# Kernel optimization log

Hardware: AMD Instinct MI355X
Metric: run time of the kernel (lower is better)

## Reference

```python
import jax, jax.numpy as jnp
import numpy as np

WH, WW = 7, 7
N = WH * WW
DIM = 384
HEADS = 12
NW = 64          # windows per image
B_ = 2048        # batch * NW


def _relative_position_index():
    ch, cw = np.meshgrid(np.arange(WH), np.arange(WW), indexing='ij')
    coords = np.stack([ch, cw]).reshape(2, -1)                      # [2, N]
    rel = coords[:, :, None] - coords[:, None, :]                   # [2, N, N]
    rel = rel.transpose(1, 2, 0)
    rel[:, :, 0] += WH - 1
    rel[:, :, 1] += WW - 1
    rel[:, :, 0] *= 2 * WW - 1
    return jnp.asarray(rel.sum(-1), dtype=jnp.int32)                # [N, N]


def setup_inputs() -> dict:
    key = jax.random.key(0)
    ks = jax.random.split(key, 7)
    return {
        'x': jax.random.normal(ks[0], (B_, N, DIM), dtype=jnp.float32),
        'qkv_w': jax.random.normal(ks[1], (3 * DIM, DIM), dtype=jnp.float32) * 0.02,
        'qkv_b': jax.random.normal(ks[2], (3 * DIM,), dtype=jnp.float32) * 0.02,
        'proj_w': jax.random.normal(ks[3], (DIM, DIM), dtype=jnp.float32) * 0.02,
        'proj_b': jax.random.normal(ks[4], (DIM,), dtype=jnp.float32) * 0.02,
        'bias_table': jax.random.normal(ks[5], ((2 * WH - 1) * (2 * WW - 1), HEADS), dtype=jnp.float32) * 0.02,
        'mask': jax.random.normal(ks[6], (NW, N, N), dtype=jnp.float32),
        'rel_idx': _relative_position_index(),
    }


def reference(x, qkv_w, qkv_b, proj_w, proj_b, bias_table, mask, rel_idx):
    B_, n, C = x.shape
    H = HEADS
    hd = C // H
    scale = hd ** (-0.5)

    qkv = x @ qkv_w.T + qkv_b                                        # [B_, N, 3C]
    qkv = qkv.reshape(B_, n, 3, H, hd).transpose(2, 0, 3, 1, 4)      # [3, B_, H, N, hd]
    q, k, v = qkv[0], qkv[1], qkv[2]

    attn = jnp.einsum('bhqd,bhkd->bhqk', q * scale, k)               # [B_, H, N, N]

    rpb = bias_table[rel_idx.reshape(-1)].reshape(n, n, H)           # gather [N, N, H]
    attn = attn + rpb.transpose(2, 0, 1)[None]                       # [B_, H, N, N]

    nW = mask.shape[0]
    attn = attn.reshape(B_ // nW, nW, H, n, n) + mask[None, :, None]
    attn = attn.reshape(B_, H, n, n)
    attn = jax.nn.softmax(attn, axis=-1)

    out = jnp.einsum('bhqk,bhkd->bhqd', attn, v)                     # [B_, H, N, hd]
    out = out.transpose(0, 2, 1, 3).reshape(B_, n, C)
    return out @ proj_w.T + proj_b
```

## Files before the change

kernel.cpp:

```cpp
#include <hip/hip_runtime.h>
#include <hip/hip_bf16.h>
#include <cstdint>
#include <cstddef>

#define NTOK 49
#define DIM 384
#define KDIM 384
#define HEADS 12
#define HD 32
#define BATCH 2048
#define MROWS (BATCH * NTOK)

typedef unsigned short u16;
typedef __bf16 bf16x8 __attribute__((ext_vector_type(8)));
typedef unsigned short u16x8 __attribute__((ext_vector_type(8)));
typedef float f32x4 __attribute__((ext_vector_type(4)));

__device__ __forceinline__ u16 f2b(float f) {
  union { float f; unsigned u; } v; v.f = f;
  unsigned r = v.u + 0x7fffu + ((v.u >> 16) & 1u);
  return (u16)(r >> 16);
}

__device__ __forceinline__ bf16x8 ld_bf8(const u16* p) {
  u16x8 u = *(const u16x8*)p;
  return __builtin_bit_cast(bf16x8, u);
}

__device__ __forceinline__ void gload_lds16(const void* g, void* l) {
  __builtin_amdgcn_global_load_lds(
      (const __attribute__((address_space(1))) unsigned*)g,
      (__attribute__((address_space(3))) unsigned*)l, 16, 0, 0);
}

__global__ __launch_bounds__(256) void k_prep(const float* __restrict__ x,
                                              u16* __restrict__ xb,
                                              const float* __restrict__ qkv_w,
                                              u16* __restrict__ wqkvb,
                                              const float* __restrict__ proj_w,
                                              u16* __restrict__ wprojb,
                                              const float* __restrict__ bias_table,
                                              const float* __restrict__ mask,
                                              const int* __restrict__ rel_idx,
                                              float* __restrict__ rpbm) {
  int blk = blockIdx.x;
  if (blk < 38208) {
    const float* in;
    u16* out;
    int i;
    if (blk < 37632) {
      in = x; out = xb; i = blk * 256 + threadIdx.x;
    } else if (blk < 38064) {
      in = qkv_w; out = wqkvb; i = (blk - 37632) * 256 + threadIdx.x;
    } else {
      in = proj_w; out = wprojb; i = (blk - 38064) * 256 + threadIdx.x;
    }
    float4 v = ((const float4*)in)[i];
    ushort4 o;
    o.x = f2b(v.x); o.y = f2b(v.y); o.z = f2b(v.z); o.w = f2b(v.w);
    ((ushort4*)out)[i] = o;
  } else {
    int idx = (blk - 38208) * 256 + threadIdx.x;
    int r  = idx & 3;
    int l  = (idx >> 2) & 63;
    int ni = (idx >> 8) & 3;
    int mi = (idx >> 10) & 3;
    int w  = (idx >> 12) & 63;
    int h  = idx >> 18;
    int kk = mi * 16 + (l >> 4) * 4 + r;
    int qq = ni * 16 + (l & 15);
    float v = -1e30f;
    if (kk < NTOK && qq < NTOK)
      v = bias_table[rel_idx[qq * NTOK + kk] * HEADS + h] +
          mask[(w * NTOK + qq) * NTOK + kk];
    rpbm[idx] = v;
  }
}

template <int OUT_BF16, int NCOLS, int NTN, int GD8>
__global__ __launch_bounds__(512, 4) void k_gemm256(const u16* __restrict__ A,
                                                    const u16* __restrict__ B,
                                                    const float* __restrict__ bias,
                                                    void* __restrict__ Cv) {
  __shared__ u16 sh[36864];
  int bid = blockIdx.x;
  int tile = (bid & 7) * GD8 + (bid >> 3);
  int mt = tile / NTN, nt = tile - mt * NTN;
  long m0 = (long)mt * 256;
  int n0 = nt * 128;
  int tid = threadIdx.x;
  int lane = tid & 63, wid = tid >> 6;
  int wr = (wid >> 1) * 64, wc = (wid & 1) * 64;
  int c = lane & 15, g = lane >> 4;
  int gsw = (g ^ ((c >> 1) & 3)) * 8;

  int srow = wid * 16 + (lane >> 2);
  int scol = ((lane & 3) ^ ((lane >> 3) & 3)) * 8;
  const u16* gA = A + (m0 + srow) * (long)KDIM + scol;
  const u16* gB = B + (long)(n0 + srow) * KDIM + scol;
  int lrow = srow, lseg = (lane & 3) * 8;

  f32x4 acc[4][4] = {};
  bf16x8 af[4], bfr[4];

#define STAGE256(BUF, KT)                                                      \
  {                                                                            \
    u16* As_ = sh + (BUF) * 12288;                                             \
    u16* Bs_ = As_ + 8192;                                                     \
    gload_lds16(gA + (KT), &As_[lrow * 32 + lseg]);                            \
    gload_lds16(gA + (KT) + 128L * KDIM, &As_[(lrow + 128) * 32 + lseg]);      \
    gload_lds16(gB + (KT), &Bs_[lrow * 32 + lseg]);                            \
  }

#define FRAGREAD(BUF)                                                          \
  {                                                                            \
    const u16* As = sh + (BUF) * 12288;                                        \
    const u16* Bs = As + 8192;                                                 \
    _Pragma("unroll") for (int i = 0; i < 4; ++i) {                            \
      af[i]  = ld_bf8(&As[(wr + i * 16 + c) * 32 + gsw]);                      \
      bfr[i] = ld_bf8(&Bs[(wc + i * 16 + c) * 32 + gsw]);                      \
    }                                                                          \
  }

#define MFMA_CL                                                                \
  __builtin_amdgcn_s_setprio(1);                                               \
  _Pragma("unroll") for (int mi = 0; mi < 4; ++mi)                             \
  _Pragma("unroll") for (int ni = 0; ni < 4; ++ni)                             \
      acc[mi][ni] = __builtin_amdgcn_mfma_f32_16x16x32_bf16(                   \
          af[mi], bfr[ni], acc[mi][ni], 0, 0, 0);                              \
  __builtin_amdgcn_s_setprio(0);

#define GITER(T, NV)                                                           \
  {                                                                            \
    MFMA_CL;                                                                   \
    asm volatile("s_waitcnt vmcnt(" #NV ")" ::: "memory");                     \
    __builtin_amdgcn_s_barrier();                                              \
    __builtin_amdgcn_sched_barrier(0);                                         \
    if ((T) + 3 < 12) STAGE256((T) % 3, ((T) + 3) * 32);                       \
    FRAGREAD(((T) + 1) % 3);                                                   \
  }

  STAGE256(0, 0);
  STAGE256(1, 32);
  STAGE256(2, 64);
  asm volatile("s_waitcnt vmcnt(6)" ::: "memory");
  __builtin_amdgcn_s_barrier();
  __builtin_amdgcn_sched_barrier(0);
  FRAGREAD(0);

  GITER(0, 3)  GITER(1, 3)  GITER(2, 3)  GITER(3, 3)
  GITER(4, 3)  GITER(5, 3)  GITER(6, 3)  GITER(7, 3)
  GITER(8, 3)  GITER(9, 3)  GITER(10, 0)
  { MFMA_CL; }
  __builtin_amdgcn_s_barrier();
#undef GITER
#undef MFMA_CL
#undef FRAGREAD
#undef STAGE256

  if (OUT_BF16) {
    u16* C = (u16*)Cv;
#pragma unroll
    for (int mi = 0; mi < 4; ++mi)
#pragma unroll
      for (int ni = 0; ni < 4; ++ni) {
        int col = wc + ni * 16 + c;
        float bv = bias[n0 + col];
#pragma unroll
        for (int r = 0; r < 4; ++r) {
          int row = wr + mi * 16 + g * 4 + r;
          sh[row * 128 + col] = f2b(acc[mi][ni][r] + bv);
        }
      }
    __syncthreads();
#pragma unroll
    for (int rep = 0; rep < 8; ++rep) {
      int idx = rep * 4096 + tid * 8;
      int row = idx >> 7, col = idx & 127;
      int grow = (int)m0 + row;
      int b = grow / 49, tok = grow - b * 49;
      int gcol = n0 + col;
      int t = gcol / 384;
      int hc = gcol - t * 384;
      int h = hc >> 5, d0 = hc & 31;
      size_t off = (((size_t)(t * 12 + h) * BATCH + b) * 49 + tok) * 32 + d0;
      *(u16x8*)(C + off) = *(const u16x8*)&sh[idx];
    }
  } else {
    float* C = (float*)Cv;
    float* shf = (float*)sh;
#pragma unroll
    for (int chunk = 0; chunk < 2; ++chunk) {
      __syncthreads();
      if ((wid >> 2) == chunk) {
#pragma unroll
        for (int mi = 0; mi < 4; ++mi)
#pragma unroll
          for (int ni = 0; ni < 4; ++ni) {
            int col = wc + ni * 16 + c;
            float bv = bias[n0 + col];
#pragma unroll
            for (int r = 0; r < 4; ++r) {
              int lr = ((wid >> 1) & 1) * 64 + mi * 16 + g * 4 + r;
              shf[lr * 128 + col] = acc[mi][ni][r] + bv;
            }
          }
      }
      __syncthreads();
#pragma unroll
      for (int rep = 0; rep < 8; ++rep) {
        int idx = rep * 2048 + tid * 4;
        int row = idx >> 7, col = idx & 127;
        *(float4*)(C + (m0 + chunk * 128 + row) * NCOLS + n0 + col) =
            *(const float4*)&shf[idx];
      }
    }
  }
}

__global__ __launch_bounds__(256) void k_attn(const u16* __restrict__ qkv,
                                              const float* __restrict__ rpbmT,
                                              u16* __restrict__ attnout) {
  __shared__ u16 P_lds[4][64 * 64];
  __shared__ u16 vT_lds[4][32 * 64];
  int lane = threadIdx.x & 63, wid = threadIdx.x >> 6;
  int blk = blockIdx.x;
  int w = blk / 96;
  int rr = blk - w * 96;
  int j = rr / 3;
  int hb = rr - j * 3;
  int b = j * 64 + w;
  int h = hb * 4 + wid;
  int c = lane & 15, g = lane >> 4;

  const u16* qh = qkv + ((size_t)(h)*BATCH + b) * (49 * 32);
  const u16* kh = qkv + ((size_t)(12 + h) * BATCH + b) * (49 * 32);
  const u16* vh = qkv + ((size_t)(24 + h) * BATCH + b) * (49 * 32);

  u16x8 vv[4];
#pragma unroll
  for (int t = 0; t < 4; ++t) {
    int idx = t * 64 + lane;
    int jj = idx >> 2, d0 = (idx & 3) * 8;
    int jr = jj < NTOK ? jj : NTOK - 1;
    vv[t] = *(const u16x8*)(vh + jr * 32 + d0);
  }
  bf16x8 kf[4], qf[4];
#pragma unroll
  for (int mi = 0; mi < 4; ++mi) {
    int row = mi * 16 + c; if (row > NTOK - 1) row = NTOK - 1;
    kf[mi] = ld_bf8(kh + row * 32 + g * 8);
  }
#pragma unroll
  for (int nj = 0; nj < 4; ++nj) {
    int row = nj * 16 + c; if (row > NTOK - 1) row = NTOK - 1;
    qf[nj] = ld_bf8(qh + row * 32 + g * 8);
  }

  u16* vt = vT_lds[wid];
#pragma unroll
  for (int t = 0; t < 4; ++t) {
    int idx = t * 64 + lane;
    int jj = idx >> 2, d0 = (idx & 3) * 8;
#pragma unroll
    for (int dd = 0; dd < 8; ++dd) {
      int d = d0 + dd;
      int byte = (d * 128 + jj * 2) ^ ((d & 7) << 4);
      *(u16*)((char*)vt + byte) = (u16)vv[t][dd];
    }
  }

  f32x4 s[4][4];
  f32x4 zf = {0.f, 0.f, 0.f, 0.f};
#pragma unroll
  for (int mi = 0; mi < 4; ++mi)
#pragma unroll
    for (int nj = 0; nj < 4; ++nj)
      s[mi][nj] = __builtin_amdgcn_mfma_f32_16x16x32_bf16(kf[mi], qf[nj], zf,
                                                          0, 0, 0);

  const float scale = 0.17677669529663687f;
  const f32x4* rp = (const f32x4*)(rpbmT + ((size_t)(h * 64 + w)) * 4096);
#pragma unroll
  for (int mi = 0; mi < 4; ++mi)
#pragma unroll
    for (int nj = 0; nj < 4; ++nj) {
      f32x4 rv = rp[(mi * 4 + nj) * 64 + lane];
#pragma unroll
      for (int r = 0; r < 4; ++r)
        s[mi][nj][r] = s[mi][nj][r] * scale + rv[r];
    }

  float inv[4];
#pragma unroll
  for (int nj = 0; nj < 4; ++nj) {
    float mx = s[0][nj][0];
#pragma unroll
    for (int mi = 0; mi < 4; ++mi)
#pragma unroll
      for (int r = 0; r < 4; ++r)
        mx = fmaxf(mx, s[mi][nj][r]);
    mx = fmaxf(mx, __shfl_xor(mx, 16));
    mx = fmaxf(mx, __shfl_xor(mx, 32));
    float sum = 0.f;
#pragma unroll
    for (int mi = 0; mi < 4; ++mi)
#pragma unroll
      for (int r = 0; r < 4; ++r) {
        float p = __expf(s[mi][nj][r] - mx);
        s[mi][nj][r] = p;
        sum += p;
      }
    sum += __shfl_xor(sum, 16);
    sum += __shfl_xor(sum, 32);
    inv[nj] = __builtin_amdgcn_rcpf(sum);
  }

  u16* pl = P_lds[wid];
#pragma unroll
  for (int mi = 0; mi < 4; ++mi)
#pragma unroll
    for (int nj = 0; nj < 4; ++nj) {
      unsigned w0, w1;
      asm("v_cvt_pk_bf16_f32 %0, %1, %2"
          : "=v"(w0) : "v"(s[mi][nj][0]), "v"(s[mi][nj][1]));
      asm("v_cvt_pk_bf16_f32 %0, %1, %2"
          : "=v"(w1) : "v"(s[mi][nj][2]), "v"(s[mi][nj][3]));
      int q = nj * 16 + c;
      int byte = (q * 128 + (mi * 16 + g * 4) * 2) ^ ((c & 7) << 4);
      uint2 val; val.x = w0; val.y = w1;
      *(uint2*)((char*)pl + byte) = val;
    }
  asm volatile("s_waitcnt lgkmcnt(0)" ::: "memory");
  __builtin_amdgcn_sched_barrier(0);

  f32x4 o[2][4] = {};
#pragma unroll
  for (int ks = 0; ks < 2; ++ks) {
    bf16x8 vb[2];
#pragma unroll
    for (int mi2 = 0; mi2 < 2; ++mi2) {
      int d = mi2 * 16 + c;
      int byte = (d * 128 + ks * 64 + g * 16) ^ ((d & 7) << 4);
      vb[mi2] = __builtin_bit_cast(bf16x8, *(const u16x8*)((const char*)vt + byte));
    }
#pragma unroll
    for (int nj = 0; nj < 4; ++nj) {
      int q = nj * 16 + c;
      int byte = (q * 128 + (ks * 32 + g * 8) * 2) ^ ((c & 7) << 4);
      bf16x8 pb = __builtin_bit_cast(bf16x8, *(const u16x8*)((const char*)pl + byte));
#pragma unroll
      for (int mi2 = 0; mi2 < 2; ++mi2)
        o[mi2][nj] = __builtin_amdgcn_mfma_f32_16x16x32_bf16(vb[mi2], pb,
                                                             o[mi2][nj], 0, 0, 0);
    }
  }

  u16* obase = attnout + (size_t)b * (NTOK * DIM) + h * HD;
#pragma unroll
  for (int mi2 = 0; mi2 < 2; ++mi2)
#pragma unroll
    for (int nj = 0; nj < 4; ++nj) {
      int q = nj * 16 + c;
      if (q < NTOK) {
#pragma unroll
        for (int r = 0; r < 4; ++r)
          obase[(size_t)q * DIM + mi2 * 16 + g * 4 + r] =
              f2b(o[mi2][nj][r] * inv[nj]);
      }
    }
}

extern "C" void kernel_launch(void* const* d_in, const int* in_sizes, int n_in,
                              void* d_out, int out_size, void* d_ws, size_t ws_size,
                              hipStream_t stream) {
  const float* x       = (const float*)d_in[0];
  const float* qkv_w   = (const float*)d_in[1];
  const float* qkv_b   = (const float*)d_in[2];
  const float* proj_w  = (const float*)d_in[3];
  const float* proj_b  = (const float*)d_in[4];
  const float* bias_tb = (const float*)d_in[5];
  const float* mask    = (const float*)d_in[6];
  const int*   rel_idx = (const int*)d_in[7];
  float* out = (float*)d_out;

  char* ws = (char*)d_ws;
  u16*   xb      = (u16*)(ws + 0);
  u16*   wqkvb   = (u16*)(ws + 77070336);
  u16*   wprojb  = (u16*)(ws + 77955072);
  float* rpbm    = (float*)(ws + 78249984);
  u16*   qkv     = (u16*)(ws + 90832896);
  u16*   attnout = (u16*)(ws + 322043904);

  k_prep<<<50496, 256, 0, stream>>>(x, xb, qkv_w, wqkvb, proj_w, wprojb,
                                    bias_tb, mask, rel_idx, rpbm);

  k_gemm256<1, 1152, 9, 441><<<3528, 512, 0, stream>>>(xb, wqkvb, qkv_b,
                                                       (void*)qkv);

  k_attn<<<6144, 256, 0, stream>>>(qkv, rpbm, attnout);

  k_gemm256<0, 384, 3, 147><<<1176, 512, 0, stream>>>(attnout, wprojb, proj_b,
                                                      (void*)out);

  (void)in_sizes; (void)n_in; (void)out_size; (void)ws_size;
}
```

Measured before the change: 339.6 us.

## Switch window attention to 32x32 MFMA and keep P in registers

The attention kernel now uses 32x32x16 bf16 MFMA tiles instead of 16x16x32 for both QK^T and PV. The softmax probabilities are converted to bf16 and rearranged across lanes with v_permlane32_swap, so they feed the PV MFMA directly instead of going through an LDS round-trip. The precomputed bias+mask layout is changed to match the new accumulator layout, and one shuffle stage drops out of the reductions. This cuts LDS traffic and shared memory use, at the cost of more registers per lane for the 16-wide accumulators.

```diff
diff --git a/kernel.cpp b/kernel.cpp
--- a/kernel.cpp
+++ b/kernel.cpp
@@ -15,6 +15,7 @@
 typedef __bf16 bf16x8 __attribute__((ext_vector_type(8)));
 typedef unsigned short u16x8 __attribute__((ext_vector_type(8)));
 typedef float f32x4 __attribute__((ext_vector_type(4)));
+typedef float f32x16 __attribute__((ext_vector_type(16)));
 
 __device__ __forceinline__ u16 f2b(float f) {
   union { float f; unsigned u; } v; v.f = f;
@@ -61,14 +62,15 @@
     ((ushort4*)out)[i] = o;
   } else {
     int idx = (blk - 38208) * 256 + threadIdx.x;
-    int r  = idx & 3;
-    int l  = (idx >> 2) & 63;
-    int ni = (idx >> 8) & 3;
-    int mi = (idx >> 10) & 3;
-    int w  = (idx >> 12) & 63;
-    int h  = idx >> 18;
-    int kk = mi * 16 + (l >> 4) * 4 + r;
-    int qq = ni * 16 + (l & 15);
+    int rl   = idx & 3;
+    int l    = (idx >> 2) & 63;
+    int rq   = (idx >> 8) & 3;
+    int tile = (idx >> 10) & 3;
+    int w    = (idx >> 12) & 63;
+    int h    = idx >> 18;
+    int mi = tile >> 1, nj = tile & 1;
+    int kk = mi * 32 + rl + 8 * rq + 4 * (l >> 5);
+    int qq = nj * 32 + (l & 31);
     float v = -1e30f;
     if (kk < NTOK && qq < NTOK)
       v = bias_table[rel_idx[qq * NTOK + kk] * HEADS + h] +
@@ -221,7 +223,6 @@
 __global__ __launch_bounds__(256) void k_attn(const u16* __restrict__ qkv,
                                               const float* __restrict__ rpbmT,
                                               u16* __restrict__ attnout) {
-  __shared__ u16 P_lds[4][64 * 64];
   __shared__ u16 vT_lds[4][32 * 64];
   int lane = threadIdx.x & 63, wid = threadIdx.x >> 6;
   int blk = blockIdx.x;
@@ -231,7 +232,7 @@
   int hb = rr - j * 3;
   int b = j * 64 + w;
   int h = hb * 4 + wid;
-  int c = lane & 15, g = lane >> 4;
+  int l31 = lane & 31, hi = lane >> 5;
 
   const u16* qh = qkv + ((size_t)(h)*BATCH + b) * (49 * 32);
   const u16* kh = qkv + ((size_t)(12 + h) * BATCH + b) * (49 * 32);
@@ -245,16 +246,20 @@
     int jr = jj < NTOK ? jj : NTOK - 1;
     vv[t] = *(const u16x8*)(vh + jr * 32 + d0);
   }
-  bf16x8 kf[4], qf[4];
-#pragma unroll
-  for (int mi = 0; mi < 4; ++mi) {
-    int row = mi * 16 + c; if (row > NTOK - 1) row = NTOK - 1;
-    kf[mi] = ld_bf8(kh + row * 32 + g * 8);
-  }
-#pragma unroll
-  for (int nj = 0; nj < 4; ++nj) {
-    int row = nj * 16 + c; if (row > NTOK - 1) row = NTOK - 1;
-    qf[nj] = ld_bf8(qh + row * 32 + g * 8);
+  bf16x8 kf[2][2], qf[2][2];
+#pragma unroll
+  for (int mi = 0; mi < 2; ++mi) {
+    int row = mi * 32 + l31; if (row > NTOK - 1) row = NTOK - 1;
+#pragma unroll
+    for (int k2 = 0; k2 < 2; ++k2)
+      kf[mi][k2] = ld_bf8(kh + row * 32 + k2 * 16 + hi * 8);
+  }
+#pragma unroll
+  for (int nj = 0; nj < 2; ++nj) {
+    int row = nj * 32 + l31; if (row > NTOK - 1) row = NTOK - 1;
+#pragma unroll
+    for (int k2 = 0; k2 < 2; ++k2)
+      qf[nj][k2] = ld_bf8(qh + row * 32 + k2 * 16 + hi * 8);
   }
 
   u16* vt = vT_lds[wid];
@@ -270,105 +275,95 @@
     }
   }
 
-  f32x4 s[4][4];
-  f32x4 zf = {0.f, 0.f, 0.f, 0.f};
-#pragma unroll
-  for (int mi = 0; mi < 4; ++mi)
-#pragma unroll
-    for (int nj = 0; nj < 4; ++nj)
-      s[mi][nj] = __builtin_amdgcn_mfma_f32_16x16x32_bf16(kf[mi], qf[nj], zf,
-                                                          0, 0, 0);
+  f32x16 s[2][2];
+  f32x16 z16 = {};
+#pragma unroll
+  for (int mi = 0; mi < 2; ++mi)
+#pragma unroll
+    for (int nj = 0; nj < 2; ++nj) {
+      s[mi][nj] = __builtin_amdgcn_mfma_f32_32x32x16_bf16(kf[mi][0], qf[nj][0],
+                                                          z16, 0, 0, 0);
+      s[mi][nj] = __builtin_amdgcn_mfma_f32_32x32x16_bf16(kf[mi][1], qf[nj][1],
+                                                          s[mi][nj], 0, 0, 0);
+    }
 
   const float scale = 0.17677669529663687f;
   const f32x4* rp = (const f32x4*)(rpbmT + ((size_t)(h * 64 + w)) * 4096);
 #pragma unroll
-  for (int mi = 0; mi < 4; ++mi)
-#pragma unroll
-    for (int nj = 0; nj < 4; ++nj) {
-      f32x4 rv = rp[(mi * 4 + nj) * 64 + lane];
-#pragma unroll
-      for (int r = 0; r < 4; ++r)
-        s[mi][nj][r] = s[mi][nj][r] * scale + rv[r];
-    }
-
-  float inv[4];
-#pragma unroll
-  for (int nj = 0; nj < 4; ++nj) {
+  for (int mi = 0; mi < 2; ++mi)
+#pragma unroll
+    for (int nj = 0; nj < 2; ++nj)
+#pragma unroll
+      for (int rq = 0; rq < 4; ++rq) {
+        f32x4 rv = rp[(mi * 2 + nj) * 256 + rq * 64 + lane];
+#pragma unroll
+        for (int rl = 0; rl < 4; ++rl)
+          s[mi][nj][rq * 4 + rl] = s[mi][nj][rq * 4 + rl] * scale + rv[rl];
+      }
+
+  float inv_[2];
+#pragma unroll
+  for (int nj = 0; nj < 2; ++nj) {
     float mx = s[0][nj][0];
 #pragma unroll
-    for (int mi = 0; mi < 4; ++mi)
-#pragma unroll
-      for (int r = 0; r < 4; ++r)
+    for (int mi = 0; mi < 2; ++mi)
+#pragma unroll
+      for (int r = 0; r < 16; ++r)
         mx = fmaxf(mx, s[mi][nj][r]);
-    mx = fmaxf(mx, __shfl_xor(mx, 16));
     mx = fmaxf(mx, __shfl_xor(mx, 32));
     float sum = 0.f;
 #pragma unroll
-    for (int mi = 0; mi < 4; ++mi)
-#pragma unroll
-      for (int r = 0; r < 4; ++r) {
+    for (int mi = 0; mi < 2; ++mi)
+#pragma unroll
+      for (int r = 0; r < 16; ++r) {
         float p = __expf(s[mi][nj][r] - mx);
         s[mi][nj][r] = p;
         sum += p;
       }
-    sum += __shfl_xor(sum, 16);
     sum += __shfl_xor(sum, 32);
-    inv[nj] = __builtin_amdgcn_rcpf(sum);
-  }
-
-  u16* pl = P_lds[wid];
-#pragma unroll
-  for (int mi = 0; mi < 4; ++mi)
-#pragma unroll
-    for (int nj = 0; nj < 4; ++nj) {
-      unsigned w0, w1;
-      asm("v_cvt_pk_bf16_f32 %0, %1, %2"
-          : "=v"(w0) : "v"(s[mi][nj][0]), "v"(s[mi][nj][1]));
-      asm("v_cvt_pk_bf16_f32 %0, %1, %2"
-          : "=v"(w1) : "v"(s[mi][nj][2]), "v"(s[mi][nj][3]));
-      int q = nj * 16 + c;
-      int byte = (q * 128 + (mi * 16 + g * 4) * 2) ^ ((c & 7) << 4);
-      uint2 val; val.x = w0; val.y = w1;
-      *(uint2*)((char*)pl + byte) = val;
-    }
+    inv_[nj] = __builtin_amdgcn_rcpf(sum);
+  }
+
   asm volatile("s_waitcnt lgkmcnt(0)" ::: "memory");
   __builtin_amdgcn_sched_barrier(0);
 
-  f32x4 o[2][4] = {};
-#pragma unroll
-  for (int ks = 0; ks < 2; ++ks) {
-    bf16x8 vb[2];
-#pragma unroll
-    for (int mi2 = 0; mi2 < 2; ++mi2) {
-      int d = mi2 * 16 + c;
-      int byte = (d * 128 + ks * 64 + g * 16) ^ ((d & 7) << 4);
-      vb[mi2] = __builtin_bit_cast(bf16x8, *(const u16x8*)((const char*)vt + byte));
-    }
-#pragma unroll
-    for (int nj = 0; nj < 4; ++nj) {
-      int q = nj * 16 + c;
-      int byte = (q * 128 + (ks * 32 + g * 8) * 2) ^ ((c & 7) << 4);
-      bf16x8 pb = __builtin_bit_cast(bf16x8, *(const u16x8*)((const char*)pl + byte));
-#pragma unroll
-      for (int mi2 = 0; mi2 < 2; ++mi2)
-        o[mi2][nj] = __builtin_amdgcn_mfma_f32_16x16x32_bf16(vb[mi2], pb,
-                                                             o[mi2][nj], 0, 0, 0);
+  f32x16 o[2] = {};
+#pragma unroll
+  for (int kk = 0; kk < 4; ++kk) {
+    int byte = (l31 * 128 + kk * 32 + hi * 16) ^ ((l31 & 7) << 4);
+    bf16x8 va = __builtin_bit_cast(bf16x8, *(const u16x8*)((const char*)vt + byte));
+#pragma unroll
+    for (int nj = 0; nj < 2; ++nj) {
+      const int mi = kk >> 1, br = (kk & 1) * 8;
+      unsigned t0, t1, t2, t3;
+      asm("v_cvt_pk_bf16_f32 %0, %1, %2"
+          : "=v"(t0) : "v"(s[mi][nj][br + 0]), "v"(s[mi][nj][br + 1]));
+      asm("v_cvt_pk_bf16_f32 %0, %1, %2"
+          : "=v"(t1) : "v"(s[mi][nj][br + 2]), "v"(s[mi][nj][br + 3]));
+      asm("v_cvt_pk_bf16_f32 %0, %1, %2"
+          : "=v"(t2) : "v"(s[mi][nj][br + 4]), "v"(s[mi][nj][br + 5]));
+      asm("v_cvt_pk_bf16_f32 %0, %1, %2"
+          : "=v"(t3) : "v"(s[mi][nj][br + 6]), "v"(s[mi][nj][br + 7]));
+      asm("v_permlane32_swap_b32 %0, %1" : "+v"(t0), "+v"(t2));
+      asm("v_permlane32_swap_b32 %0, %1" : "+v"(t1), "+v"(t3));
+      uint4 uu; uu.x = t0; uu.y = t1; uu.z = t2; uu.w = t3;
+      bf16x8 pb = __builtin_bit_cast(bf16x8, uu);
+      o[nj] = __builtin_amdgcn_mfma_f32_32x32x16_bf16(va, pb, o[nj], 0, 0, 0);
     }
   }
 
   u16* obase = attnout + (size_t)b * (NTOK * DIM) + h * HD;
 #pragma unroll
-  for (int mi2 = 0; mi2 < 2; ++mi2)
-#pragma unroll
-    for (int nj = 0; nj < 4; ++nj) {
-      int q = nj * 16 + c;
-      if (q < NTOK) {
-#pragma unroll
-        for (int r = 0; r < 4; ++r)
-          obase[(size_t)q * DIM + mi2 * 16 + g * 4 + r] =
-              f2b(o[mi2][nj][r] * inv[nj]);
-      }
-    }
+  for (int nj = 0; nj < 2; ++nj) {
+    int q = nj * 32 + l31;
+    if (q < NTOK) {
+#pragma unroll
+      for (int r = 0; r < 16; ++r) {
+        int d = (r & 3) + 8 * (r >> 2) + 4 * hi;
+        obase[(size_t)q * DIM + d] = f2b(o[nj][r] * inv_[nj]);
+      }
+    }
+  }
 }
 
 extern "C" void kernel_launch(void* const* d_in, const int* in_sizes, int n_in,
```

After: 340.9 us. No clear change (+0.4%).
